# Optimization experiments

Measured on AMD Instinct MI355X. Metric: run time of the kernel, lower is better.

The kernel has to match this reference:

```python
import jax, jax.numpy as jnp
import numpy as np

SCALE_FACTORS = (0.5, 1.0)
ITERATIONS = (2, 2)
TAU = (1.0, 1.0)
SIGMA = (1.0, 1.0)
SIGMA_CUTOFF = 3.0
EPS = 1e-9
DHW = ('NCDHW', 'OIDHW', 'NCDHW')


def gaussian_kernel1d(sigma):
    radius = int(round(sigma * SIGMA_CUTOFF))
    x = np.arange(-radius, radius + 1, dtype=np.float32)
    k = np.exp(-0.5 * (x / sigma) ** 2)
    return jnp.asarray(k / k.sum())


def smooth3d(vf, kernel):
    # separable depthwise Gaussian over the 3 spatial axes; vf: (B,C,D,H,W)
    C = vf.shape[1]
    n = kernel.shape[0]
    for axis in range(3):
        shape = [1, 1, 1]
        shape[axis] = n
        kern = jnp.broadcast_to(kernel.reshape(1, 1, *shape), (C, 1, *shape))
        vf = jax.lax.conv_general_dilated(vf, kern, (1, 1, 1), 'SAME',
                                          feature_group_count=C, dimension_numbers=DHW)
    return vf


def resize_tri(x, spatial):
    return jax.image.resize(x, x.shape[:2] + tuple(spatial), method='trilinear')


def warp(img, flow):
    # trilinear grid-sample with voxel-space displacement, border clamping
    B, C, D, H, W = img.shape
    gz, gy, gx = jnp.meshgrid(jnp.arange(D, dtype=img.dtype),
                              jnp.arange(H, dtype=img.dtype),
                              jnp.arange(W, dtype=img.dtype), indexing='ij')
    base = jnp.stack([gz, gy, gx])  # (3,D,H,W)

    def one(im, fl):
        z = jnp.clip(base[0] + fl[0], 0.0, D - 1)
        y = jnp.clip(base[1] + fl[1], 0.0, H - 1)
        x = jnp.clip(base[2] + fl[2], 0.0, W - 1)
        z0 = jnp.floor(z); y0 = jnp.floor(y); x0 = jnp.floor(x)
        wz = z - z0; wy = y - y0; wx = x - x0
        z0i = z0.astype(jnp.int32); y0i = y0.astype(jnp.int32); x0i = x0.astype(jnp.int32)
        z1i = jnp.minimum(z0i + 1, D - 1)
        y1i = jnp.minimum(y0i + 1, H - 1)
        x1i = jnp.minimum(x0i + 1, W - 1)

        def g(zi, yi, xi):
            return im[:, zi, yi, xi]  # (C,D,H,W)

        return (g(z0i, y0i, x0i) * (1 - wz) * (1 - wy) * (1 - wx)
                + g(z0i, y0i, x1i) * (1 - wz) * (1 - wy) * wx
                + g(z0i, y1i, x0i) * (1 - wz) * wy * (1 - wx)
                + g(z0i, y1i, x1i) * (1 - wz) * wy * wx
                + g(z1i, y0i, x0i) * wz * (1 - wy) * (1 - wx)
                + g(z1i, y0i, x1i) * wz * (1 - wy) * wx
                + g(z1i, y1i, x0i) * wz * wy * (1 - wx)
                + g(z1i, y1i, x1i) * wz * wy * wx)

    return jax.vmap(one)(img, flow)


def demon_forces(warped, fixed):
    # 'active' demon forces: gradient of the warped moving image
    diff = warped - fixed                                  # (B,1,D,H,W)
    g = jnp.stack(jnp.gradient(warped[:, 0], axis=(1, 2, 3)), axis=1)  # (B,3,D,H,W)
    denom = jnp.sum(g * g, axis=1, keepdims=True) + diff * diff + EPS
    return diff * g / denom


def conv3(x, w, b=None):
    y = jax.lax.conv_general_dilated(x, w, (1, 1, 1), 'SAME', dimension_numbers=DHW)
    return y if b is None else y + b.reshape(1, -1, 1, 1, 1)


def inorm(x):  # InstanceNorm3d, affine=False, eps=1e-5
    m = x.mean(axis=(2, 3, 4), keepdims=True)
    v = x.var(axis=(2, 3, 4), keepdims=True)
    return (x - m) * jax.lax.rsqrt(v + 1e-5)


def mish(x):
    return x * jnp.tanh(jax.nn.softplus(x))


def updater(x, w1, w2, w3, w4, b4):
    x = mish(inorm(conv3(x, w1)))
    x = mish(inorm(conv3(x, w2)))
    x = mish(inorm(conv3(x, w3)))
    return conv3(x, w4, b4)


def match_vf(vf, spatial):
    old = vf.shape[2:]
    if tuple(old) == tuple(spatial):
        return vf
    vf2 = resize_tri(vf, spatial)
    scale = jnp.array([s1 / s2 for s1, s2 in zip(spatial, old)], dtype=vf.dtype)
    return vf2 * scale.reshape(1, 3, 1, 1, 1)


def registration(image, moving, w1, w2, w3, w4, b4):
    vf = None
    for i, (sf, iters) in enumerate(zip(SCALE_FACTORS, ITERATIONS)):
        spatial = tuple(int(s * sf) for s in image.shape[2:])
        si = resize_tri(image, spatial)
        smov = resize_tri(moving, spatial)
        vf = jnp.zeros((image.shape[0], 3) + spatial, image.dtype) if vf is None else match_vf(vf, spatial)
        kernel = gaussian_kernel1d(SIGMA[i]).astype(image.dtype)
        for _ in range(iters):
            warped = warp(smov, vf)
            forces = demon_forces(warped, si)
            feat = jnp.concatenate([forces, si, warped], axis=1)  # 5 channels
            vf = vf + TAU[i] * updater(feat, w1, w2, w3, w4, b4)
            vf = smooth3d(vf, kernel)
    vf = match_vf(vf, image.shape[2:])
    warped_full = warp(moving, vf)
    return warped_full, vf


def setup_inputs() -> dict:
    key = jax.random.key(0)
    ks = jax.random.split(key, 8)
    D = H = W = 96
    return {
        'image': jax.random.uniform(ks[0], (1, 1, D, H, W), jnp.float32),
        'mask': jnp.ones((1, 1, D, H, W), jnp.float32),
        'moving': jax.random.uniform(ks[1], (1, 1, D, H, W), jnp.float32),
        'spacing': jnp.ones((3,), jnp.float32),
        'w1': jax.random.normal(ks[2], (32, 5, 3, 3, 3), jnp.float32) * 0.05,
        'w2': jax.random.normal(ks[3], (64, 32, 3, 3, 3), jnp.float32) * 0.05,
        'w3': jax.random.normal(ks[4], (32, 64, 3, 3, 3), jnp.float32) * 0.05,
        'w4': jax.random.normal(ks[5], (3, 32, 3, 3, 3), jnp.float32) * 0.05,
        'b4': jnp.zeros((3,), jnp.float32),
    }


def reference(image, mask, moving, spacing, w1, w2, w3, w4, b4):
    # mask only feeds metrics/early-stopping (disabled: early_stopping_fn='none');
    # spacing unused since use_image_spacing=False.
    return registration(image, moving, w1, w2, w3, w4, b4)
```

## Files before the change

kernel.cpp:

```cpp
#include <hip/hip_runtime.h>
#include <hip/hip_bf16.h>


#define DEV __device__ __forceinline__
typedef __hip_bfloat16 bf16;
typedef __attribute__((ext_vector_type(8))) short short8;
typedef __attribute__((ext_vector_type(4))) float f32x4;

DEV float bfu(unsigned int u) {
  union { unsigned int i; float f; } x; x.i = u << 16; return x.f;
}
DEV unsigned short fbf(float f) {
  __hip_bfloat16 h = __float2bfloat16(f);
  return __builtin_bit_cast(unsigned short, h);
}

__global__ void zero_k(float* __restrict__ p, int n) {
  int i = blockIdx.x * 256 + threadIdx.x;
  if (i < n) p[i] = 0.f;
}
__global__ void copy_k(const float* __restrict__ in, float* __restrict__ out, int n) {
  int i = blockIdx.x * 256 + threadIdx.x;
  if (i < n) out[i] = in[i];
}

__global__ void pack_wf_k(const float* __restrict__ w, bf16* __restrict__ dst,
                          int NWT, int KB, int COR, int CIR) {
  int idx = blockIdx.x * 256 + threadIdx.x;
  int tot = 27 * NWT * KB * 512;
  if (idx >= tot) return;
  int j = idx & 7;
  int lane = (idx >> 3) & 63;
  int frag = idx >> 9;
  int kb = frag % KB;
  int r2 = frag / KB;
  int nwt = r2 % NWT;
  int off = r2 / NWT;
  int lid = lane & 15, kg = lane >> 4;
  int co = nwt * 16 + lid;
  int ci = (kb * 4 + kg) * 8 + j;
  float v = (co < COR && ci < CIR) ? w[((size_t)co * CIR + ci) * 27 + off] : 0.f;
  dst[idx] = __float2bfloat16(v);
}

DEV int ds_taps(int i, int n_out, int* j0, float* w) {
  if (i == 0) { *j0 = 0; w[0] = 3.f/7.f; w[1] = 3.f/7.f; w[2] = 1.f/7.f; return 3; }
  if (i == n_out - 1) { *j0 = 2*i - 1; w[0] = 1.f/7.f; w[1] = 3.f/7.f; w[2] = 3.f/7.f; return 3; }
  *j0 = 2*i - 1; w[0] = 0.125f; w[1] = 0.375f; w[2] = 0.375f; w[3] = 0.125f; return 4;
}
DEV void up_taps(int i, int n_in, int* j0, int* j1, float* w0, float* w1) {
  if (i & 1) {
    int k = i >> 1;
    if (k + 1 >= n_in) { *j0 = n_in - 1; *j1 = n_in - 1; *w0 = 1.f; *w1 = 0.f; }
    else { *j0 = k; *j1 = k + 1; *w0 = 0.75f; *w1 = 0.25f; }
  } else {
    int k = i >> 1;
    if (k == 0) { *j0 = 0; *j1 = 0; *w0 = 1.f; *w1 = 0.f; }
    else { *j0 = k - 1; *j1 = k; *w0 = 0.25f; *w1 = 0.75f; }
  }
}

__global__ void down2x_k(const float* __restrict__ in, float* __restrict__ out,
                         int Do, int Ho, int Wo) {
  const int Hi = 2 * Ho, Wi = 2 * Wo;
  const int No = Do * Ho * Wo;
  int i = blockIdx.x * 256 + threadIdx.x;
  if (i >= No) return;
  int xo = i % Wo; int t = i / Wo; int yo = t % Ho; int zo = t / Ho;
  int jz0, jy0, jx0; float wz[4], wy[4], wx[4];
  int cz = ds_taps(zo, Do, &jz0, wz);
  int cy = ds_taps(yo, Ho, &jy0, wy);
  int cx = ds_taps(xo, Wo, &jx0, wx);
  float s = 0.f;
  for (int a = 0; a < cz; ++a) {
    const float* pz = in + (size_t)(jz0 + a) * Hi * Wi;
    for (int b = 0; b < cy; ++b) {
      const float* py = pz + (size_t)(jy0 + b) * Wi;
      float wab = wz[a] * wy[b];
      for (int d = 0; d < cx; ++d) s += wab * wx[d] * py[jx0 + d];
    }
  }
  out[i] = s;
}

__global__ void up2x_vf_k(const float* __restrict__ in, float* __restrict__ out,
                          int Do, int Ho, int Wo) {
  const int Di = Do / 2, Hi = Ho / 2, Wi = Wo / 2;
  const int No = Do * Ho * Wo;
  const int c = blockIdx.y;
  int i = blockIdx.x * 256 + threadIdx.x;
  if (i >= No) return;
  int xo = i % Wo; int t = i / Wo; int yo = t % Ho; int zo = t / Ho;
  int jz0, jz1, jy0, jy1, jx0, jx1; float wz0, wz1, wy0, wy1, wx0, wx1;
  up_taps(zo, Di, &jz0, &jz1, &wz0, &wz1);
  up_taps(yo, Hi, &jy0, &jy1, &wy0, &wy1);
  up_taps(xo, Wi, &jx0, &jx1, &wx0, &wx1);
  const float* p = in + (size_t)c * Di * Hi * Wi;
  float v00 = wx0 * p[(jz0 * Hi + jy0) * Wi + jx0] + wx1 * p[(jz0 * Hi + jy0) * Wi + jx1];
  float v01 = wx0 * p[(jz0 * Hi + jy1) * Wi + jx0] + wx1 * p[(jz0 * Hi + jy1) * Wi + jx1];
  float v10 = wx0 * p[(jz1 * Hi + jy0) * Wi + jx0] + wx1 * p[(jz1 * Hi + jy0) * Wi + jx1];
  float v11 = wx0 * p[(jz1 * Hi + jy1) * Wi + jx0] + wx1 * p[(jz1 * Hi + jy1) * Wi + jx1];
  float s = wz0 * (wy0 * v00 + wy1 * v01) + wz1 * (wy0 * v10 + wy1 * v11);
  out[(size_t)c * No + i] = 2.f * s;
}

__global__ void warp_k(const float* __restrict__ img, const float* __restrict__ vf,
                       float* __restrict__ out, int D, int H, int W) {
  const int N = D * H * W;
  int i = blockIdx.x * 256 + threadIdx.x;
  if (i >= N) return;
  int x = i % W; int t = i / W; int y = t % H; int z = t / H;
  float zc = fminf(fmaxf((float)z + vf[i], 0.f), (float)(D - 1));
  float yc = fminf(fmaxf((float)y + vf[(size_t)N + i], 0.f), (float)(H - 1));
  float xc = fminf(fmaxf((float)x + vf[2 * (size_t)N + i], 0.f), (float)(W - 1));
  float zf = floorf(zc), yf = floorf(yc), xf = floorf(xc);
  int z0 = (int)zf, y0 = (int)yf, x0 = (int)xf;
  float wz = zc - zf, wy = yc - yf, wx = xc - xf;
  int z1 = min(z0 + 1, D - 1), y1 = min(y0 + 1, H - 1), x1 = min(x0 + 1, W - 1);
  const int HW = H * W;
  float v000 = img[z0 * HW + y0 * W + x0];
  float v001 = img[z0 * HW + y0 * W + x1];
  float v010 = img[z0 * HW + y1 * W + x0];
  float v011 = img[z0 * HW + y1 * W + x1];
  float v100 = img[z1 * HW + y0 * W + x0];
  float v101 = img[z1 * HW + y0 * W + x1];
  float v110 = img[z1 * HW + y1 * W + x0];
  float v111 = img[z1 * HW + y1 * W + x1];
  float r = v000 * (1 - wz) * (1 - wy) * (1 - wx)
          + v001 * (1 - wz) * (1 - wy) * wx
          + v010 * (1 - wz) * wy * (1 - wx)
          + v011 * (1 - wz) * wy * wx
          + v100 * wz * (1 - wy) * (1 - wx)
          + v101 * wz * (1 - wy) * wx
          + v110 * wz * wy * (1 - wx)
          + v111 * wz * wy * wx;
  out[i] = r;
}

__global__ void forces8_k(const float* __restrict__ wpd, const float* __restrict__ si,
                          bf16* __restrict__ feat, int D, int H, int W) {
  const int N = D * H * W;
  int i = blockIdx.x * 256 + threadIdx.x;
  if (i >= N) return;
  int x = i % W; int t = i / W; int y = t % H; int z = t / H;
  float wv = wpd[i];
  const int HW = H * W;
  float gz = (z == 0) ? (wpd[i + HW] - wv) : (z == D - 1) ? (wv - wpd[i - HW]) : 0.5f * (wpd[i + HW] - wpd[i - HW]);
  float gy = (y == 0) ? (wpd[i + W] - wv) : (y == H - 1) ? (wv - wpd[i - W]) : 0.5f * (wpd[i + W] - wpd[i - W]);
  float gx = (x == 0) ? (wpd[i + 1] - wv) : (x == W - 1) ? (wv - wpd[i - 1]) : 0.5f * (wpd[i + 1] - wpd[i - 1]);
  float s = si[i];
  float diff = wv - s;
  float denom = gz * gz + gy * gy + gx * gx + diff * diff + 1e-9f;
  short8 o;
  o[0] = (short)fbf((diff * gz) / denom);
  o[1] = (short)fbf((diff * gy) / denom);
  o[2] = (short)fbf((diff * gx) / denom);
  o[3] = (short)fbf(s);
  o[4] = (short)fbf(wv);
  o[5] = 0; o[6] = 0; o[7] = 0;
  *(short8*)((short*)feat + (size_t)i * 8) = o;
}

template <int CIN, int COUT, int TZ, int TY, int INS, int REDUCE>
__global__ void __launch_bounds__(512) convmf_k(
    const bf16* __restrict__ act, const bf16* __restrict__ wpk,
    bf16* __restrict__ out, double* __restrict__ pbuf, int D, int H, int W) {
  constexpr int CH = CIN / 8;
  constexpr int HZ = TZ + 2, HY = TY + 2;
  constexpr int HALO = HZ * HY * 18;
  constexpr int MS = TZ * TY / 4;
  constexpr int NS = COUT / 32;
  constexpr int NWT = COUT / 16;
  constexpr int KB = CIN / 32;
  __shared__ short lds[HALO * CIN];
  __shared__ float2 red[8][NS][16];
  const int t = threadIdx.x;
  const int gx0 = blockIdx.x * 16, gy0 = blockIdx.y * TY, gz0 = blockIdx.z * TZ;
  const short* actS = (const short*)act;
  for (int cid = t; cid < HALO * CH; cid += 512) {
    int pos = cid / CH, c = cid - pos * CH;
    int hx = pos % 18; int r = pos / 18; int hy = r % HY; int hz = r / HY;
    int gz = gz0 + hz - 1, gy = gy0 + hy - 1, gx = gx0 + hx - 1;
    uint4 v = {0u, 0u, 0u, 0u};
    if (((unsigned)gz < (unsigned)D) & ((unsigned)gy < (unsigned)H) & ((unsigned)gx < (unsigned)W)) {
      size_t vox = (size_t)(gz * H + gy) * W + gx;
      if (INS == 8) { if (c == 0) v = *(const uint4*)(actS + vox * 8); }
      else v = *(const uint4*)(actS + vox * CIN + c * 8);
    }
    *(uint4*)(lds + pos * CIN + ((c ^ (pos & (CH - 1))) * 8)) = v;
  }
  __syncthreads();
  const int lane = t & 63, wid = t >> 6;
  const int mw = wid & 3, nw = wid >> 2;
  const int lid = lane & 15, kg = lane >> 4;
  f32x4 acc[MS][NS];
#pragma unroll
  for (int ms = 0; ms < MS; ++ms)
#pragma unroll
    for (int n = 0; n < NS; ++n) acc[ms][n] = {0.f, 0.f, 0.f, 0.f};
  int rowpos[MS];
#pragma unroll
  for (int ms = 0; ms < MS; ++ms) {
    int r = mw * MS + ms;
    rowpos[ms] = ((r / TY) * HY + (r % TY)) * 18 + lid;
  }
  const short* wp = (const short*)wpk;
#pragma unroll 1
  for (int kz = 0; kz < 3; ++kz)
#pragma unroll 1
    for (int ky = 0; ky < 3; ++ky) {
      const int delta0 = (kz * HY + ky) * 18;
#pragma unroll
      for (int kx = 0; kx < 3; ++kx) {
        const int off = (kz * 3 + ky) * 3 + kx;
        short8 bq[NS][KB];
#pragma unroll
        for (int n = 0; n < NS; ++n)
#pragma unroll
          for (int kb = 0; kb < KB; ++kb)
            bq[n][kb] = *(const short8*)(wp + ((((size_t)off * NWT + nw * NS + n) * KB + kb) << 9) + lane * 8);
#pragma unroll
        for (int ms = 0; ms < MS; ++ms) {
          int pos = rowpos[ms] + delta0 + kx;
          int sw = pos & (CH - 1);
#pragma unroll
          for (int kb = 0; kb < KB; ++kb) {
            short8 a = *(const short8*)(lds + pos * CIN + (((kb * 4 + kg) ^ sw) * 8));
#pragma unroll
            for (int n = 0; n < NS; ++n)
              acc[ms][n] = __builtin_amdgcn_mfma_f32_16x16x32_bf16(a, bq[n][kb], acc[ms][n], 0, 0, 0);
          }
        }
      }
    }
  const int xe = kg * 4;
#pragma unroll
  for (int ms = 0; ms < MS; ++ms) {
    int r = mw * MS + ms;
    int z = gz0 + r / TY, y = gy0 + r % TY;
    size_t voxb = (size_t)(z * H + y) * W + gx0;
#pragma unroll
    for (int n = 0; n < NS; ++n) {
      int co = nw * NS * 16 + n * 16 + lid;
#pragma unroll
      for (int rg = 0; rg < 4; ++rg)
        out[(voxb + xe + rg) * COUT + co] = __float2bfloat16(acc[ms][n][rg]);
    }
  }
  if (REDUCE) {
#pragma unroll
    for (int n = 0; n < NS; ++n) {
      float s = 0.f, q = 0.f;
#pragma unroll
      for (int ms = 0; ms < MS; ++ms)
#pragma unroll
        for (int rg = 0; rg < 4; ++rg) {
          float v = acc[ms][n][rg];
          s += v; q += v * v;
        }
      s += __shfl_xor(s, 16); q += __shfl_xor(q, 16);
      s += __shfl_xor(s, 32); q += __shfl_xor(q, 32);
      if (lane < 16) red[wid][n][lane] = make_float2(s, q);
    }
    __syncthreads();
    if (t < COUT) {
      const int nw_ = t / (NS * 16);
      const int rem = t - nw_ * NS * 16;
      const int n_ = rem >> 4, lid_ = rem & 15;
      float S = 0.f, Q = 0.f;
#pragma unroll
      for (int m = 0; m < 4; ++m) {
        float2 v = red[nw_ * 4 + m][n_][lid_];
        S += v.x; Q += v.y;
      }
      const int G = gridDim.x * gridDim.y * gridDim.z;
      const int bid = blockIdx.x + gridDim.x * (blockIdx.y + gridDim.y * blockIdx.z);
      pbuf[((size_t)t * G + bid) * 2 + 0] = (double)S;
      pbuf[((size_t)t * G + bid) * 2 + 1] = (double)Q;
    }
  }
}

template <int TZ, int TY>
__global__ void __launch_bounds__(512) conv4mf_k(
    const bf16* __restrict__ act, const bf16* __restrict__ wpk,
    const float* __restrict__ bias, float* __restrict__ vf, int D, int H, int W) {
  constexpr int CH = 4;
  constexpr int HZ = TZ + 2, HY = TY + 2;
  constexpr int HALO = HZ * HY * 18;
  constexpr int MS = TZ * TY / 8;
  __shared__ short lds[HALO * 32];
  const int t = threadIdx.x;
  const int gx0 = blockIdx.x * 16, gy0 = blockIdx.y * TY, gz0 = blockIdx.z * TZ;
  const int N = D * H * W;
  const short* actS = (const short*)act;
  for (int cid = t; cid < HALO * CH; cid += 512) {
    int pos = cid / CH, c = cid - pos * CH;
    int hx = pos % 18; int r = pos / 18; int hy = r % HY; int hz = r / HY;
    int gz = gz0 + hz - 1, gy = gy0 + hy - 1, gx = gx0 + hx - 1;
    uint4 v = {0u, 0u, 0u, 0u};
    if (((unsigned)gz < (unsigned)D) & ((unsigned)gy < (unsigned)H) & ((unsigned)gx < (unsigned)W))
      v = *(const uint4*)(actS + ((size_t)(gz * H + gy) * W + gx) * 32 + c * 8);
    *(uint4*)(lds + pos * 32 + ((c ^ (pos & 3)) * 8)) = v;
  }
  __syncthreads();
  const int lane = t & 63, wid = t >> 6;
  const int lid = lane & 15, kg = lane >> 4;
  f32x4 acc[MS];
#pragma unroll
  for (int ms = 0; ms < MS; ++ms) acc[ms] = {0.f, 0.f, 0.f, 0.f};
  int rowpos[MS];
#pragma unroll
  for (int ms = 0; ms < MS; ++ms) {
    int r = wid * MS + ms;
    rowpos[ms] = ((r / TY) * HY + (r % TY)) * 18 + lid;
  }
  const short* wp = (const short*)wpk;
#pragma unroll 1
  for (int kz = 0; kz < 3; ++kz)
#pragma unroll 1
    for (int ky = 0; ky < 3; ++ky) {
      const int delta0 = (kz * HY + ky) * 18;
#pragma unroll
      for (int kx = 0; kx < 3; ++kx) {
        const int off = (kz * 3 + ky) * 3 + kx;
        short8 b = *(const short8*)(wp + ((size_t)off << 9) + lane * 8);
#pragma unroll
        for (int ms = 0; ms < MS; ++ms) {
          int pos = rowpos[ms] + delta0 + kx;
          int sw = pos & 3;
          short8 a = *(const short8*)(lds + pos * 32 + ((kg ^ sw) * 8));
          acc[ms] = __builtin_amdgcn_mfma_f32_16x16x32_bf16(a, b, acc[ms], 0, 0, 0);
        }
      }
    }
  if (lid < 3) {
    float bs = bias[lid];
#pragma unroll
    for (int ms = 0; ms < MS; ++ms) {
      int r = wid * MS + ms;
      int z = gz0 + r / TY, y = gy0 + r % TY;
      size_t voxb = (size_t)(z * H + y) * W + gx0 + kg * 4;
      float* p = vf + (size_t)lid * N + voxb;
#pragma unroll
      for (int rg = 0; rg < 4; ++rg) p[rg] += acc[ms][rg] + bs;
    }
  }
}

__global__ void stage2_k(const double* __restrict__ pbuf, float2* __restrict__ musc,
                         int N, int G) {
  const int c = blockIdx.x;
  double S = 0, Q = 0;
  for (int g = threadIdx.x; g < G; g += 256) {
    S += pbuf[((size_t)c * G + g) * 2 + 0];
    Q += pbuf[((size_t)c * G + g) * 2 + 1];
  }
  for (int off = 32; off > 0; off >>= 1) {
    S += __shfl_down(S, off); Q += __shfl_down(Q, off);
  }
  __shared__ double ls[4], lq[4];
  const int wid = threadIdx.x >> 6, lane = threadIdx.x & 63;
  if (lane == 0) { ls[wid] = S; lq[wid] = Q; }
  __syncthreads();
  if (threadIdx.x == 0) {
    double St = ls[0] + ls[1] + ls[2] + ls[3];
    double Qt = lq[0] + lq[1] + lq[2] + lq[3];
    double m = St / N;
    double var = Qt / N - m * m;
    musc[c] = make_float2((float)m, (float)(1.0 / sqrt(var + 1e-5)));
  }
}

DEV float mishf(float v) {
  if (v > 20.f) return v;
  float u = __expf(v);
  float w = u * (u + 2.f);
  return v * (w / (w + 2.f));
}

template <int C>
__global__ void inorm_vc_k(bf16* __restrict__ x, const float2* __restrict__ musc, int N) {
  constexpr int CP = C / 2;
  constexpr int VPB = 256 / CP;
  const int cp = threadIdx.x & (CP - 1);
  const int vt = threadIdx.x / CP;
  float2 m0 = musc[2 * cp], m1 = musc[2 * cp + 1];
  unsigned int* p = (unsigned int*)x;
  int v0 = blockIdx.x * (4 * VPB) + vt;
#pragma unroll
  for (int r = 0; r < 4; ++r) {
    int v = v0 + r * VPB;
    size_t idx = (size_t)v * CP + cp;
    unsigned int u = p[idx];
    float a = mishf((bfu(u & 0xffffu) - m0.x) * m0.y);
    float b = mishf((bfu(u >> 16) - m1.x) * m1.y);
    p[idx] = (unsigned int)fbf(a) | ((unsigned int)fbf(b) << 16);
  }
}

template <int AXIS>
__global__ void smooth_k(const float* __restrict__ in, float* __restrict__ out,
                         int D, int H, int W) {
  const int N = D * H * W;
  const int c = blockIdx.y;
  int i = blockIdx.x * 256 + threadIdx.x;
  if (i >= N) return;
  int x = i % W; int t = i / W; int y = t % H; int z = t / H;
  const int coord = AXIS == 0 ? z : AXIS == 1 ? y : x;
  const int len = AXIS == 0 ? D : AXIS == 1 ? H : W;
  const int stride = AXIS == 0 ? H * W : AXIS == 1 ? W : 1;
  const float k1 = 0.60653065971263342f, k2 = 0.13533528323661270f, k3 = 0.011108996538242306f;
  const float kn = 1.f / (1.f + 2.f * (k1 + k2 + k3));
  const float gw[4] = {kn, k1 * kn, k2 * kn, k3 * kn};
  const float* p = in + (size_t)c * N;
  float s = gw[0] * p[i];
#pragma unroll
  for (int tt = 1; tt <= 3; ++tt) {
    if (coord - tt >= 0) s += gw[tt] * p[i - tt * stride];
    if (coord + tt < len) s += gw[tt] * p[i + tt * stride];
  }
  out[(size_t)c * N + i] = s;
}

extern "C" void kernel_launch(void* const* d_in, const int* in_sizes, int n_in,
                              void* d_out, int out_size, void* d_ws, size_t ws_size,
                              hipStream_t stream) {
  const float* image  = (const float*)d_in[0];
  const float* moving = (const float*)d_in[2];
  const float* w1 = (const float*)d_in[4];
  const float* w2 = (const float*)d_in[5];
  const float* w3 = (const float*)d_in[6];
  const float* w4 = (const float*)d_in[7];
  const float* b4 = (const float*)d_in[8];
  float* out = (float*)d_out;

  const int D1 = 96; const int N1 = D1 * D1 * D1;
  const int D0 = 48; const int N0 = D0 * D0 * D0;

  char* wsp = (char*)d_ws;
  double* pbuf  = (double*)wsp;          wsp += (size_t)64 * 13824 * 2 * 8;
  float2* musc  = (float2*)wsp;          wsp += 1024;
  bf16* w1p     = (bf16*)wsp;            wsp += 27 * 2 * 1 * 512 * 2;
  bf16* w2p     = (bf16*)wsp;            wsp += 27 * 4 * 1 * 512 * 2;
  bf16* w3p     = (bf16*)wsp;            wsp += 27 * 2 * 2 * 512 * 2;
  bf16* w4p     = (bf16*)wsp;            wsp += 27 * 1 * 1 * 512 * 2;
  float* si0    = (float*)wsp;           wsp += (size_t)N0 * 4;
  float* smov0  = (float*)wsp;           wsp += (size_t)N0 * 4;
  float* vf0    = (float*)wsp;           wsp += 3 * (size_t)N1 * 4;
  float* vf1    = (float*)wsp;           wsp += 3 * (size_t)N1 * 4;
  float* warped = (float*)wsp;           wsp += (size_t)N1 * 4;
  bf16* feat    = (bf16*)wsp;            wsp += 8 * (size_t)N1 * 2;
  bf16* bufA    = (bf16*)wsp;            wsp += 32 * (size_t)N1 * 2;
  bf16* bufB    = (bf16*)wsp;            wsp += 64 * (size_t)N1 * 2;

  pack_wf_k<<<(27 * 2 * 512 + 255) / 256, 256, 0, stream>>>(w1, w1p, 2, 1, 32, 5);
  pack_wf_k<<<(27 * 4 * 512 + 255) / 256, 256, 0, stream>>>(w2, w2p, 4, 1, 64, 32);
  pack_wf_k<<<(27 * 4 * 512 + 255) / 256, 256, 0, stream>>>(w3, w3p, 2, 2, 32, 64);
  pack_wf_k<<<(27 * 1 * 512 + 255) / 256, 256, 0, stream>>>(w4, w4p, 1, 1, 3, 32);

  down2x_k<<<N0 / 256, 256, 0, stream>>>(image, si0, D0, D0, D0);
  down2x_k<<<N0 / 256, 256, 0, stream>>>(moving, smov0, D0, D0, D0);
  zero_k<<<3 * N0 / 256, 256, 0, stream>>>(vf0, 3 * N0);

  float* vfc = vf0;
  float* vfa = vf1;

  auto run_level = [&](const float* si, const float* smov, int Dd) {
    const int N = Dd * Dd * Dd;
    const int nb = N / 256;
    const dim3 g1(Dd / 16, Dd / 4, Dd / 4);
    const dim3 g3(Dd / 16, Dd / 4, Dd / 2);
    const int G1 = g1.x * g1.y * g1.z;
    const int G3 = g3.x * g3.y * g3.z;
    for (int it = 0; it < 2; ++it) {
      warp_k<<<nb, 256, 0, stream>>>(smov, vfc, warped, Dd, Dd, Dd);
      forces8_k<<<nb, 256, 0, stream>>>(warped, si, feat, Dd, Dd, Dd);

      convmf_k<32, 32, 4, 4, 8, 1><<<g1, 512, 0, stream>>>(feat, w1p, bufA, pbuf, Dd, Dd, Dd);
      stage2_k<<<32, 256, 0, stream>>>(pbuf, musc, N, G1);
      inorm_vc_k<32><<<N / 64, 256, 0, stream>>>(bufA, musc, N);

      convmf_k<32, 64, 4, 4, 32, 1><<<g1, 512, 0, stream>>>(bufA, w2p, bufB, pbuf, Dd, Dd, Dd);
      stage2_k<<<64, 256, 0, stream>>>(pbuf, musc, N, G1);
      inorm_vc_k<64><<<N / 32, 256, 0, stream>>>(bufB, musc, N);

      convmf_k<64, 32, 2, 4, 64, 1><<<g3, 512, 0, stream>>>(bufB, w3p, bufA, pbuf, Dd, Dd, Dd);
      stage2_k<<<32, 256, 0, stream>>>(pbuf, musc, N, G3);
      inorm_vc_k<32><<<N / 64, 256, 0, stream>>>(bufA, musc, N);

      conv4mf_k<4, 4><<<g1, 512, 0, stream>>>(bufA, w4p, b4, vfc, Dd, Dd, Dd);

      smooth_k<0><<<dim3(nb, 3), 256, 0, stream>>>(vfc, vfa, Dd, Dd, Dd);
      smooth_k<1><<<dim3(nb, 3), 256, 0, stream>>>(vfa, vfc, Dd, Dd, Dd);
      smooth_k<2><<<dim3(nb, 3), 256, 0, stream>>>(vfc, vfa, Dd, Dd, Dd);
      { float* tmp = vfc; vfc = vfa; vfa = tmp; }
    }
  };

  run_level(si0, smov0, D0);

  up2x_vf_k<<<dim3(N1 / 256, 3), 256, 0, stream>>>(vfc, vfa, D1, D1, D1);
  { float* tmp = vfc; vfc = vfa; vfa = tmp; }

  run_level(image, moving, D1);

  warp_k<<<N1 / 256, 256, 0, stream>>>(moving, vfc, out, D1, D1, D1);
  copy_k<<<3 * N1 / 256, 256, 0, stream>>>(vfc, out + N1, 3 * N1);
}
```

Before: 1.353 ms.

## Fuse instance-norm+Mish into next conv's halo load and merge warp with forces

Removes the separate in-place instance-norm/Mish passes by applying normalization and Mish while loading each activation into the next convolution's shared-memory halo. Warp and force computation are combined into one tiled kernel that warps a halo region into shared memory and takes gradients from it, which drops the intermediate warped buffer. This saves a full read-write pass over bufA/bufB per layer and several kernel launches. In exchange, halo voxels are normalized redundantly across neighbouring blocks, and the warp kernel recomputes warps for halo cells.

```diff
diff --git a/kernel.cpp b/kernel.cpp
--- a/kernel.cpp
+++ b/kernel.cpp
@@ -13,6 +13,13 @@
 DEV unsigned short fbf(float f) {
   __hip_bfloat16 h = __float2bfloat16(f);
   return __builtin_bit_cast(unsigned short, h);
+}
+
+DEV float mishf(float v) {
+  if (v > 20.f) return v;
+  float u = __expf(v);
+  float w = u * (u + 2.f);
+  return v * (w / (w + 2.f));
 }
 
 __global__ void zero_k(float* __restrict__ p, int n) {
@@ -36,9 +43,8 @@
   int r2 = frag / KB;
   int nwt = r2 % NWT;
   int off = r2 / NWT;
-  int lid = lane & 15, kg = lane >> 4;
-  int co = nwt * 16 + lid;
-  int ci = (kb * 4 + kg) * 8 + j;
+  int co = nwt * 16 + (lane & 15);
+  int ci = (kb * 4 + (lane >> 4)) * 8 + j;
   float v = (co < COR && ci < CIR) ? w[((size_t)co * CIR + ci) * 27 + off] : 0.f;
   dst[idx] = __float2bfloat16(v);
 }
@@ -104,15 +110,11 @@
   out[(size_t)c * No + i] = 2.f * s;
 }
 
-__global__ void warp_k(const float* __restrict__ img, const float* __restrict__ vf,
-                       float* __restrict__ out, int D, int H, int W) {
-  const int N = D * H * W;
-  int i = blockIdx.x * 256 + threadIdx.x;
-  if (i >= N) return;
-  int x = i % W; int t = i / W; int y = t % H; int z = t / H;
+DEV float warp1(const float* __restrict__ img, const float* __restrict__ vf,
+                int x, int y, int z, size_t i, int D, int H, int W, size_t N) {
   float zc = fminf(fmaxf((float)z + vf[i], 0.f), (float)(D - 1));
-  float yc = fminf(fmaxf((float)y + vf[(size_t)N + i], 0.f), (float)(H - 1));
-  float xc = fminf(fmaxf((float)x + vf[2 * (size_t)N + i], 0.f), (float)(W - 1));
+  float yc = fminf(fmaxf((float)y + vf[N + i], 0.f), (float)(H - 1));
+  float xc = fminf(fmaxf((float)x + vf[2 * N + i], 0.f), (float)(W - 1));
   float zf = floorf(zc), yf = floorf(yc), xf = floorf(xc);
   int z0 = (int)zf, y0 = (int)yf, x0 = (int)xf;
   float wz = zc - zf, wy = yc - yf, wx = xc - xf;
@@ -126,28 +128,51 @@
   float v101 = img[z1 * HW + y0 * W + x1];
   float v110 = img[z1 * HW + y1 * W + x0];
   float v111 = img[z1 * HW + y1 * W + x1];
-  float r = v000 * (1 - wz) * (1 - wy) * (1 - wx)
-          + v001 * (1 - wz) * (1 - wy) * wx
-          + v010 * (1 - wz) * wy * (1 - wx)
-          + v011 * (1 - wz) * wy * wx
-          + v100 * wz * (1 - wy) * (1 - wx)
-          + v101 * wz * (1 - wy) * wx
-          + v110 * wz * wy * (1 - wx)
-          + v111 * wz * wy * wx;
-  out[i] = r;
-}
-
-__global__ void forces8_k(const float* __restrict__ wpd, const float* __restrict__ si,
-                          bf16* __restrict__ feat, int D, int H, int W) {
-  const int N = D * H * W;
-  int i = blockIdx.x * 256 + threadIdx.x;
+  return v000 * (1 - wz) * (1 - wy) * (1 - wx)
+       + v001 * (1 - wz) * (1 - wy) * wx
+       + v010 * (1 - wz) * wy * (1 - wx)
+       + v011 * (1 - wz) * wy * wx
+       + v100 * wz * (1 - wy) * (1 - wx)
+       + v101 * wz * (1 - wy) * wx
+       + v110 * wz * wy * (1 - wx)
+       + v111 * wz * wy * wx;
+}
+
+__global__ void warp_k(const float* __restrict__ img, const float* __restrict__ vf,
+                       float* __restrict__ out, int D, int H, int W) {
+  const size_t N = (size_t)D * H * W;
+  size_t i = (size_t)blockIdx.x * 256 + threadIdx.x;
   if (i >= N) return;
   int x = i % W; int t = i / W; int y = t % H; int z = t / H;
-  float wv = wpd[i];
-  const int HW = H * W;
-  float gz = (z == 0) ? (wpd[i + HW] - wv) : (z == D - 1) ? (wv - wpd[i - HW]) : 0.5f * (wpd[i + HW] - wpd[i - HW]);
-  float gy = (y == 0) ? (wpd[i + W] - wv) : (y == H - 1) ? (wv - wpd[i - W]) : 0.5f * (wpd[i + W] - wpd[i - W]);
-  float gx = (x == 0) ? (wpd[i + 1] - wv) : (x == W - 1) ? (wv - wpd[i - 1]) : 0.5f * (wpd[i + 1] - wpd[i - 1]);
+  out[i] = warp1(img, vf, x, y, z, i, D, H, W, N);
+}
+
+__global__ void __launch_bounds__(256) warpforce_k(
+    const float* __restrict__ img, const float* __restrict__ vf,
+    const float* __restrict__ si, bf16* __restrict__ feat, int D, int H, int W) {
+  __shared__ float wt[600];
+  const size_t N = (size_t)D * H * W;
+  const int t = threadIdx.x;
+  const int tx = t & 7, ty = (t >> 3) & 7, tz = t >> 6;
+  const int gx0 = blockIdx.x * 8, gy0 = blockIdx.y * 8, gz0 = blockIdx.z * 4;
+  for (int cid = t; cid < 600; cid += 256) {
+    int hx = cid % 10; int r = cid / 10; int hy = r % 10; int hz = r / 10;
+    int gz = gz0 + hz - 1, gy = gy0 + hy - 1, gx = gx0 + hx - 1;
+    float w = 0.f;
+    if (((unsigned)gz < (unsigned)D) & ((unsigned)gy < (unsigned)H) & ((unsigned)gx < (unsigned)W)) {
+      size_t i = (size_t)(gz * H + gy) * W + gx;
+      w = warp1(img, vf, gx, gy, gz, i, D, H, W, N);
+    }
+    wt[cid] = w;
+  }
+  __syncthreads();
+  const int x = gx0 + tx, y = gy0 + ty, z = gz0 + tz;
+  const size_t i = (size_t)(z * H + y) * W + x;
+  const int c = (tz + 1) * 100 + (ty + 1) * 10 + (tx + 1);
+  float wv = wt[c];
+  float gz = (z == 0) ? (wt[c + 100] - wv) : (z == D - 1) ? (wv - wt[c - 100]) : 0.5f * (wt[c + 100] - wt[c - 100]);
+  float gy = (y == 0) ? (wt[c + 10] - wv) : (y == H - 1) ? (wv - wt[c - 10]) : 0.5f * (wt[c + 10] - wt[c - 10]);
+  float gx = (x == 0) ? (wt[c + 1] - wv) : (x == W - 1) ? (wv - wt[c - 1]) : 0.5f * (wt[c + 1] - wt[c - 1]);
   float s = si[i];
   float diff = wv - s;
   float denom = gz * gz + gy * gy + gx * gx + diff * diff + 1e-9f;
@@ -158,13 +183,14 @@
   o[3] = (short)fbf(s);
   o[4] = (short)fbf(wv);
   o[5] = 0; o[6] = 0; o[7] = 0;
-  *(short8*)((short*)feat + (size_t)i * 8) = o;
-}
-
-template <int CIN, int COUT, int TZ, int TY, int INS, int REDUCE>
+  *(short8*)((short*)feat + i * 8) = o;
+}
+
+template <int CIN, int COUT, int TZ, int TY, int INS, int REDUCE, int NORM>
 __global__ void __launch_bounds__(512) convmf_k(
     const bf16* __restrict__ act, const bf16* __restrict__ wpk,
-    bf16* __restrict__ out, double* __restrict__ pbuf, int D, int H, int W) {
+    const float2* __restrict__ musc, bf16* __restrict__ out,
+    double* __restrict__ pbuf, int D, int H, int W) {
   constexpr int CH = CIN / 8;
   constexpr int HZ = TZ + 2, HY = TY + 2;
   constexpr int HALO = HZ * HY * 18;
@@ -185,7 +211,18 @@
     if (((unsigned)gz < (unsigned)D) & ((unsigned)gy < (unsigned)H) & ((unsigned)gx < (unsigned)W)) {
       size_t vox = (size_t)(gz * H + gy) * W + gx;
       if (INS == 8) { if (c == 0) v = *(const uint4*)(actS + vox * 8); }
-      else v = *(const uint4*)(actS + vox * CIN + c * 8);
+      else {
+        v = *(const uint4*)(actS + vox * CIN + c * 8);
+        if (NORM) {
+          short* sp = (short*)&v;
+#pragma unroll
+          for (int j = 0; j < 8; ++j) {
+            float2 mm = musc[c * 8 + j];
+            float f = mishf((bfu((unsigned short)sp[j]) - mm.x) * mm.y);
+            sp[j] = (short)fbf(f);
+          }
+        }
+      }
     }
     *(uint4*)(lds + pos * CIN + ((c ^ (pos & (CH - 1))) * 8)) = v;
   }
@@ -284,7 +321,8 @@
 template <int TZ, int TY>
 __global__ void __launch_bounds__(512) conv4mf_k(
     const bf16* __restrict__ act, const bf16* __restrict__ wpk,
-    const float* __restrict__ bias, float* __restrict__ vf, int D, int H, int W) {
+    const float2* __restrict__ musc, const float* __restrict__ bias,
+    float* __restrict__ vf, int D, int H, int W) {
   constexpr int CH = 4;
   constexpr int HZ = TZ + 2, HY = TY + 2;
   constexpr int HALO = HZ * HY * 18;
@@ -299,8 +337,16 @@
     int hx = pos % 18; int r = pos / 18; int hy = r % HY; int hz = r / HY;
     int gz = gz0 + hz - 1, gy = gy0 + hy - 1, gx = gx0 + hx - 1;
     uint4 v = {0u, 0u, 0u, 0u};
-    if (((unsigned)gz < (unsigned)D) & ((unsigned)gy < (unsigned)H) & ((unsigned)gx < (unsigned)W))
+    if (((unsigned)gz < (unsigned)D) & ((unsigned)gy < (unsigned)H) & ((unsigned)gx < (unsigned)W)) {
       v = *(const uint4*)(actS + ((size_t)(gz * H + gy) * W + gx) * 32 + c * 8);
+      short* sp = (short*)&v;
+#pragma unroll
+      for (int j = 0; j < 8; ++j) {
+        float2 mm = musc[c * 8 + j];
+        float f = mishf((bfu((unsigned short)sp[j]) - mm.x) * mm.y);
+        sp[j] = (short)fbf(f);
+      }
+    }
     *(uint4*)(lds + pos * 32 + ((c ^ (pos & 3)) * 8)) = v;
   }
   __syncthreads();
@@ -369,33 +415,6 @@
     double m = St / N;
     double var = Qt / N - m * m;
     musc[c] = make_float2((float)m, (float)(1.0 / sqrt(var + 1e-5)));
-  }
-}
-
-DEV float mishf(float v) {
-  if (v > 20.f) return v;
-  float u = __expf(v);
-  float w = u * (u + 2.f);
-  return v * (w / (w + 2.f));
-}
-
-template <int C>
-__global__ void inorm_vc_k(bf16* __restrict__ x, const float2* __restrict__ musc, int N) {
-  constexpr int CP = C / 2;
-  constexpr int VPB = 256 / CP;
-  const int cp = threadIdx.x & (CP - 1);
-  const int vt = threadIdx.x / CP;
-  float2 m0 = musc[2 * cp], m1 = musc[2 * cp + 1];
-  unsigned int* p = (unsigned int*)x;
-  int v0 = blockIdx.x * (4 * VPB) + vt;
-#pragma unroll
-  for (int r = 0; r < 4; ++r) {
-    int v = v0 + r * VPB;
-    size_t idx = (size_t)v * CP + cp;
-    unsigned int u = p[idx];
-    float a = mishf((bfu(u & 0xffffu) - m0.x) * m0.y);
-    float b = mishf((bfu(u >> 16) - m1.x) * m1.y);
-    p[idx] = (unsigned int)fbf(a) | ((unsigned int)fbf(b) << 16);
   }
 }
 
@@ -449,7 +468,6 @@
   float* smov0  = (float*)wsp;           wsp += (size_t)N0 * 4;
   float* vf0    = (float*)wsp;           wsp += 3 * (size_t)N1 * 4;
   float* vf1    = (float*)wsp;           wsp += 3 * (size_t)N1 * 4;
-  float* warped = (float*)wsp;           wsp += (size_t)N1 * 4;
   bf16* feat    = (bf16*)wsp;            wsp += 8 * (size_t)N1 * 2;
   bf16* bufA    = (bf16*)wsp;            wsp += 32 * (size_t)N1 * 2;
   bf16* bufB    = (bf16*)wsp;            wsp += 64 * (size_t)N1 * 2;
@@ -469,27 +487,24 @@
   auto run_level = [&](const float* si, const float* smov, int Dd) {
     const int N = Dd * Dd * Dd;
     const int nb = N / 256;
+    const dim3 gw(Dd / 8, Dd / 8, Dd / 4);
     const dim3 g1(Dd / 16, Dd / 4, Dd / 4);
     const dim3 g3(Dd / 16, Dd / 4, Dd / 2);
     const int G1 = g1.x * g1.y * g1.z;
     const int G3 = g3.x * g3.y * g3.z;
     for (int it = 0; it < 2; ++it) {
-      warp_k<<<nb, 256, 0, stream>>>(smov, vfc, warped, Dd, Dd, Dd);
-      forces8_k<<<nb, 256, 0, stream>>>(warped, si, feat, Dd, Dd, Dd);
-
-      convmf_k<32, 32, 4, 4, 8, 1><<<g1, 512, 0, stream>>>(feat, w1p, bufA, pbuf, Dd, Dd, Dd);
+      warpforce_k<<<gw, 256, 0, stream>>>(smov, vfc, si, feat, Dd, Dd, Dd);
+
+      convmf_k<32, 32, 4, 4, 8, 1, 0><<<g1, 512, 0, stream>>>(feat, w1p, musc, bufA, pbuf, Dd, Dd, Dd);
       stage2_k<<<32, 256, 0, stream>>>(pbuf, musc, N, G1);
-      inorm_vc_k<32><<<N / 64, 256, 0, stream>>>(bufA, musc, N);
-
-      convmf_k<32, 64, 4, 4, 32, 1><<<g1, 512, 0, stream>>>(bufA, w2p, bufB, pbuf, Dd, Dd, Dd);
+
+      convmf_k<32, 64, 4, 4, 32, 1, 1><<<g1, 512, 0, stream>>>(bufA, w2p, musc, bufB, pbuf, Dd, Dd, Dd);
       stage2_k<<<64, 256, 0, stream>>>(pbuf, musc, N, G1);
-      inorm_vc_k<64><<<N / 32, 256, 0, stream>>>(bufB, musc, N);
-
-      convmf_k<64, 32, 2, 4, 64, 1><<<g3, 512, 0, stream>>>(bufB, w3p, bufA, pbuf, Dd, Dd, Dd);
+
+      convmf_k<64, 32, 2, 4, 64, 1, 1><<<g3, 512, 0, stream>>>(bufB, w3p, musc, bufA, pbuf, Dd, Dd, Dd);
       stage2_k<<<32, 256, 0, stream>>>(pbuf, musc, N, G3);
-      inorm_vc_k<32><<<N / 64, 256, 0, stream>>>(bufA, musc, N);
-
-      conv4mf_k<4, 4><<<g1, 512, 0, stream>>>(bufA, w4p, b4, vfc, Dd, Dd, Dd);
+
+      conv4mf_k<4, 4><<<g1, 512, 0, stream>>>(bufA, w4p, musc, b4, vfc, Dd, Dd, Dd);
 
       smooth_k<0><<<dim3(nb, 3), 256, 0, stream>>>(vfc, vfa, Dd, Dd, Dd);
       smooth_k<1><<<dim3(nb, 3), 256, 0, stream>>>(vfa, vfc, Dd, Dd, Dd);
```

Measured after the change: 1.728 ms. 1.28x slower.
